# Performance work log

Measured on AMD Instinct MI355X. Metric: run time of the kernel, lower is better.

Reference implementation:

```python
import jax, jax.numpy as jnp
import numpy as np

G, N, E = 64, 1000, 8192          # graphs, nodes/graph, edges/graph
F_IN, C, H, HID, NCLS = 128, 128, 4, 256, 2
EPS = 1e-5


def _gcn(x, src, dst, W, b):
    # GCNConv: symmetric normalization with self-loops, sum aggregation.
    h = x @ W                                              # [N, C]
    deg = jax.ops.segment_sum(jnp.ones(E, h.dtype), dst, num_segments=N) + 1.0
    dinv = jax.lax.rsqrt(deg)                              # deg^{-1/2}
    msg = h[src] * (dinv[src] * dinv[dst])[:, None]        # [E, C] gather
    out = jax.ops.segment_sum(msg, dst, num_segments=N)    # scatter-add
    out = out + h * (dinv * dinv)[:, None]                 # self-loop term
    return out + b


def _layernorm(y, g, b):
    mu = y.mean(-1, keepdims=True)
    var = ((y - mu) ** 2).mean(-1, keepdims=True)
    return (y - mu) * jax.lax.rsqrt(var + EPS) * g + b


def setup_inputs() -> dict:
    key = jax.random.key(0)
    ks = jax.random.split(key, 12)
    rn = lambda k, s: jax.random.normal(k, s, jnp.float32) * 0.05
    return dict(
        x=jax.random.normal(ks[0], (G, N, F_IN), jnp.float32),
        edge_index=jax.random.randint(ks[1], (G, 2, E), 0, N),
        W0=rn(ks[2], (F_IN, C)), b0=jnp.zeros((C,), jnp.float32),
        W1=rn(ks[3], (C, C)), b1=jnp.zeros((C,), jnp.float32),
        in_w=rn(ks[4], (3 * C, C)), in_b=jnp.zeros((3 * C,), jnp.float32),
        out_w=rn(ks[5], (C, C)), out_b=jnp.zeros((C,), jnp.float32),
        ln2_g=jnp.ones((C,), jnp.float32), ln2_b=jnp.zeros((C,), jnp.float32),
        mw1=rn(ks[6], (C, HID)), mb1=jnp.zeros((HID,), jnp.float32),
        mw2=rn(ks[7], (HID, C)), mb2=jnp.zeros((C,), jnp.float32),
        lw=rn(ks[8], (C, NCLS)), lb=jnp.zeros((NCLS,), jnp.float32),
    )


def reference(x, edge_index, W0, b0, W1, b1, in_w, in_b, out_w, out_b,
              ln2_g, ln2_b, mw1, mb1, mw2, mb2, lw, lb):
    src, dst = edge_index[:, 0, :], edge_index[:, 1, :]
    conv = jax.vmap(_gcn, in_axes=(0, 0, 0, None, None))
    h = jnp.tanh(conv(x, src, dst, W0, b0))   # [G, N, C]
    h = jnp.tanh(conv(h, src, dst, W1, b1))
    g = h.sum(axis=1)                          # SumAggregation -> [G, C]

    # MultiheadAttention, unbatched: sequence of G graph embeddings
    qkv = g @ in_w.T + in_b
    q, k, v = jnp.split(qkv, 3, axis=-1)
    d = C // H
    qh, kh, vh = (t.reshape(G, H, d) for t in (q, k, v))
    attn = jax.nn.softmax(jnp.einsum('qhd,khd->hqk', qh, kh) * (d ** -0.5), axis=-1)
    o = jnp.einsum('hqk,khd->qhd', attn, vh).reshape(G, C) @ out_w.T + out_b

    x_attend = o                               # dropout = identity (eval)
    # NOTE: original computes layer_norm1(x_attend) but immediately overwrites it.
    mlp = jnp.maximum(x_attend @ mw1 + mb1, 0.0) @ mw2 + mb2
    y = _layernorm(x_attend + mlp, ln2_g, ln2_b)
    node_repr = jnp.maximum(y, 0.0).sum(axis=0)  # [C]
    return node_repr @ lw + lb                   # [NCLS]
```

## Files before the change

kernel.cpp:

```cpp
#include <hip/hip_runtime.h>
#include <math.h>

#define Gn 64
#define Nn 1000
#define En 8192
#define Cc 128
#define HIDn 256
#define EPSf 1e-5f

typedef __attribute__((ext_vector_type(8))) short bh8;
typedef __attribute__((ext_vector_type(4))) float fx4;

__device__ __forceinline__ unsigned short f2bf(float f) {
    unsigned u = __float_as_uint(f);
    u += 0x7fffu + ((u >> 16) & 1u);
    return (unsigned short)(u >> 16);
}
__device__ __forceinline__ float bflo(unsigned u) { return __uint_as_float(u << 16); }
__device__ __forceinline__ float bfhi(unsigned u) { return __uint_as_float(u & 0xffff0000u); }

__global__ __launch_bounds__(256) void k_fused(const int* __restrict__ ei, const float* __restrict__ X,
                                               const float* __restrict__ W, int4* __restrict__ ninfo,
                                               int2* __restrict__ epair, float* __restrict__ pooled,
                                               float* __restrict__ repr, int* __restrict__ ctr,
                                               unsigned short* __restrict__ Hout)
{
    __shared__ __align__(16) short Wt[128][136];
    __shared__ int   curs[1024];
    __shared__ float dinv_s[1024];
    __shared__ int   wsum[4];
    int t = threadIdx.x;

    if (blockIdx.x >= 256) {
        int g = blockIdx.x - 256;
        const int* srcp = ei + (size_t)g * 2 * En;
        const int* dstp = srcp + En;
        int lane = t & 63, wv = t >> 6;

        #pragma unroll
        for (int j = 0; j < 4; ++j) curs[t * 4 + j] = 0;
        __syncthreads();
        for (int e = t; e < En; e += 256) atomicAdd(&curs[dstp[e]], 1);
        __syncthreads();

        int base = t * 4;
        int d0 = curs[base], d1 = curs[base + 1], d2 = curs[base + 2], d3 = curs[base + 3];
        int s = d0 + d1 + d2 + d3;
        int v = s;
        #pragma unroll
        for (int off = 1; off <= 32; off <<= 1) {
            int u = __shfl_up(v, off);
            if (lane >= off) v += u;
        }
        if (lane == 63) wsum[wv] = v;
        __syncthreads();
        int woff = 0;
        #pragma unroll
        for (int w = 0; w < 4; ++w) if (w < wv) woff += wsum[w];
        int e0 = woff + v - s;
        int e1 = e0 + d0, e2 = e1 + d1, e3 = e2 + d2;
        float dv0 = rsqrtf((float)d0 + 1.f), dv1 = rsqrtf((float)d1 + 1.f);
        float dv2 = rsqrtf((float)d2 + 1.f), dv3 = rsqrtf((float)d3 + 1.f);
        curs[base] = e0; curs[base + 1] = e1; curs[base + 2] = e2; curs[base + 3] = e3;
        dinv_s[base] = dv0; dinv_s[base + 1] = dv1; dinv_s[base + 2] = dv2; dinv_s[base + 3] = dv3;
        if (base < Nn)     ninfo[g * Nn + base]     = make_int4(e0, d0, __float_as_int(dv0 * dv0), 0);
        if (base + 1 < Nn) ninfo[g * Nn + base + 1] = make_int4(e1, d1, __float_as_int(dv1 * dv1), 0);
        if (base + 2 < Nn) ninfo[g * Nn + base + 2] = make_int4(e2, d2, __float_as_int(dv2 * dv2), 0);
        if (base + 3 < Nn) ninfo[g * Nn + base + 3] = make_int4(e3, d3, __float_as_int(dv3 * dv3), 0);
        __syncthreads();

        for (int e = t; e < En; e += 256) {
            int dd = dstp[e], ss = srcp[e];
            int p = atomicAdd(&curs[dd], 1);
            float w = dinv_s[ss] * dinv_s[dd];
            epair[(size_t)g * En + p] = make_int2(ss, __float_as_int(w));
        }
        if (t < Cc) pooled[g * Cc + t] = 0.f;
        if (g == 0 && t < Cc) repr[t] = 0.f;
        if (g == 0 && t == 0) *ctr = 0;
        return;
    }

    int b = blockIdx.x;
    int xcd = b & 7, j = b >> 3;
    int g = xcd + 8 * (j & 7);
    int rblk = j >> 3;
    for (int idx = t; idx < 16384; idx += 256) {
        int kI = idx >> 7, n = idx & 127;
        Wt[n][kI] = (short)f2bf(W[idx]);
    }
    __syncthreads();
    int wave = t >> 6, l = t & 63;
    int lr = l & 15, lg = l >> 4;
    const float* Xf = X + (size_t)g * Nn * Cc;
    unsigned short* Hg = Hout + (size_t)g * Nn * Cc;

    for (int s = 0; s < 4; ++s) {
        int rbase = rblk * 256 + wave * 64 + s * 16;
        int r = rbase + lr;
        bool ok = r < Nn;
        bh8 af[4];
        #pragma unroll
        for (int ks = 0; ks < 4; ++ks) {
            if (ok) {
                const float* xp = Xf + (size_t)r * Cc + ks * 32 + lg * 8;
                fx4 a0 = *(const fx4*)xp;
                fx4 a1 = *(const fx4*)(xp + 4);
                bh8 av;
                av[0] = (short)f2bf(a0[0]); av[1] = (short)f2bf(a0[1]);
                av[2] = (short)f2bf(a0[2]); av[3] = (short)f2bf(a0[3]);
                av[4] = (short)f2bf(a1[0]); av[5] = (short)f2bf(a1[1]);
                av[6] = (short)f2bf(a1[2]); av[7] = (short)f2bf(a1[3]);
                af[ks] = av;
            } else af[ks] = bh8{0, 0, 0, 0, 0, 0, 0, 0};
        }
        fx4 acc[8];
        #pragma unroll
        for (int ct = 0; ct < 8; ++ct) acc[ct] = fx4{0.f, 0.f, 0.f, 0.f};
        #pragma unroll
        for (int ks = 0; ks < 4; ++ks) {
            #pragma unroll
            for (int ct = 0; ct < 8; ++ct) {
                bh8 bfr = *(const bh8*)(&Wt[ct * 16 + lr][ks * 32 + lg * 8]);
                acc[ct] = __builtin_amdgcn_mfma_f32_16x16x32_bf16(af[ks], bfr, acc[ct], 0, 0, 0);
            }
        }
        #pragma unroll
        for (int ct = 0; ct < 8; ++ct) {
            #pragma unroll
            for (int rg = 0; rg < 4; ++rg) {
                int row = rbase + lg * 4 + rg;
                if (row < Nn) Hg[(size_t)row * Cc + ct * 16 + lr] = f2bf(acc[ct][rg]);
            }
        }
    }
}

__global__ __launch_bounds__(256) void k_gemm1(const unsigned short* __restrict__ Xh,
                                               const float* __restrict__ W,
                                               unsigned short* __restrict__ Hout)
{
    __shared__ __align__(16) short Wt[128][136];
    int b = blockIdx.x;
    int xcd = b & 7, j = b >> 3;
    int g = xcd + 8 * (j & 7);
    int rblk = j >> 3;
    int t = threadIdx.x;
    for (int idx = t; idx < 16384; idx += 256) {
        int kI = idx >> 7, n = idx & 127;
        Wt[n][kI] = (short)f2bf(W[idx]);
    }
    __syncthreads();
    int wave = t >> 6, l = t & 63;
    int lr = l & 15, lg = l >> 4;
    const short* Xg = (const short*)Xh + (size_t)g * Nn * Cc;
    unsigned short* Hg = Hout + (size_t)g * Nn * Cc;

    for (int s = 0; s < 4; ++s) {
        int rbase = rblk * 256 + wave * 64 + s * 16;
        int r = rbase + lr;
        bool ok = r < Nn;
        bh8 af[4];
        #pragma unroll
        for (int ks = 0; ks < 4; ++ks) {
            if (ok) af[ks] = *(const bh8*)(Xg + (size_t)r * Cc + ks * 32 + lg * 8);
            else    af[ks] = bh8{0, 0, 0, 0, 0, 0, 0, 0};
        }
        fx4 acc[8];
        #pragma unroll
        for (int ct = 0; ct < 8; ++ct) acc[ct] = fx4{0.f, 0.f, 0.f, 0.f};
        #pragma unroll
        for (int ks = 0; ks < 4; ++ks) {
            #pragma unroll
            for (int ct = 0; ct < 8; ++ct) {
                bh8 bfr = *(const bh8*)(&Wt[ct * 16 + lr][ks * 32 + lg * 8]);
                acc[ct] = __builtin_amdgcn_mfma_f32_16x16x32_bf16(af[ks], bfr, acc[ct], 0, 0, 0);
            }
        }
        #pragma unroll
        for (int ct = 0; ct < 8; ++ct) {
            #pragma unroll
            for (int rg = 0; rg < 4; ++rg) {
                int row = rbase + lg * 4 + rg;
                if (row < Nn) Hg[(size_t)row * Cc + ct * 16 + lr] = f2bf(acc[ct][rg]);
            }
        }
    }
}

template<int POOL>
__global__ __launch_bounds__(256) void k_combine(const unsigned* __restrict__ Hb, const int2* __restrict__ epair,
                                                 const int4* __restrict__ ninfo, const float* __restrict__ bias,
                                                 unsigned* __restrict__ Tout, float* __restrict__ pooled)
{
    int b = blockIdx.x;
    int xcd = b & 7, j = b >> 3;
    int g = xcd + 8 * (j & 7);
    int blk = j >> 3;
    int wave = threadIdx.x >> 6, lane = threadIdx.x & 63;
    const unsigned* Hg = Hb + (size_t)g * Nn * 64;
    const int2* epg = epair + (size_t)g * En;
    const int4* nig = ninfo + (size_t)g * Nn;
    float2 bb = *(const float2*)(bias + lane * 2);
    float px = 0.f, py = 0.f;
    for (int n = blk * 4 + wave; n < Nn; n += 128) {
        int4 ni = nig[n];
        int st = ni.x, dc = ni.y;
        float sw = __int_as_float(ni.z);
        unsigned hv = Hg[n * 64 + lane];
        float a0x = bflo(hv) * sw + bb.x, a0y = bfhi(hv) * sw + bb.y;
        float a1x = 0.f, a1y = 0.f, a2x = 0.f, a2y = 0.f, a3x = 0.f, a3y = 0.f;
        int e = 0;
        for (; e + 4 <= dc; e += 4) {
            int2 p0 = epg[st + e];
            int2 p1 = epg[st + e + 1];
            int2 p2 = epg[st + e + 2];
            int2 p3 = epg[st + e + 3];
            unsigned r0 = Hg[p0.x * 64 + lane];
            unsigned r1 = Hg[p1.x * 64 + lane];
            unsigned r2 = Hg[p2.x * 64 + lane];
            unsigned r3 = Hg[p3.x * 64 + lane];
            float w0 = __int_as_float(p0.y), w1 = __int_as_float(p1.y);
            float w2 = __int_as_float(p2.y), w3 = __int_as_float(p3.y);
            a0x = fmaf(bflo(r0), w0, a0x); a0y = fmaf(bfhi(r0), w0, a0y);
            a1x = fmaf(bflo(r1), w1, a1x); a1y = fmaf(bfhi(r1), w1, a1y);
            a2x = fmaf(bflo(r2), w2, a2x); a2y = fmaf(bfhi(r2), w2, a2y);
            a3x = fmaf(bflo(r3), w3, a3x); a3y = fmaf(bfhi(r3), w3, a3y);
        }
        for (; e < dc; ++e) {
            int2 p0 = epg[st + e];
            unsigned r0 = Hg[p0.x * 64 + lane];
            float w0 = __int_as_float(p0.y);
            a0x = fmaf(bflo(r0), w0, a0x); a0y = fmaf(bfhi(r0), w0, a0y);
        }
        float ax = (a0x + a1x) + (a2x + a3x);
        float ay = (a0y + a1y) + (a2y + a3y);
        float tx = tanhf(ax), ty = tanhf(ay);
        if (POOL) { px += tx; py += ty; }
        else Tout[(size_t)(g * Nn + n) * 64 + lane] = ((unsigned)f2bf(ty) << 16) | (unsigned)f2bf(tx);
    }
    if (POOL) {
        atomicAdd(&pooled[g * Cc + lane * 2], px);
        atomicAdd(&pooled[g * Cc + lane * 2 + 1], py);
    }
}

__global__ __launch_bounds__(1024) void k_qkv(const float* __restrict__ pooled, const float* __restrict__ in_w,
                                              const float* __restrict__ in_b, float* __restrict__ qkvb)
{
    int t = threadIdx.x, lane = t & 63, wv = t >> 6;
    int c = blockIdx.x * 16 + wv;
    const float* wr = in_w + c * Cc;
    float w0 = wr[lane], w1 = wr[64 + lane];
    float bias = in_b[c];
    for (int i = 0; i < Gn; ++i) {
        float p = fmaf(pooled[i * Cc + lane], w0, pooled[i * Cc + 64 + lane] * w1);
        #pragma unroll
        for (int off2 = 32; off2 > 0; off2 >>= 1) p += __shfl_xor(p, off2);
        if (lane == 0) qkvb[i * 384 + c] = p + bias;
    }
}

__global__ __launch_bounds__(1024) void k_attn(const float* __restrict__ qkvb, float* __restrict__ ob)
{
    __shared__ float q[64][33], kk[64][33], v[64][33];
    __shared__ float S[64][64];
    int h = blockIdx.x, t = threadIdx.x;

    for (int idx = t; idx < 2048; idx += 1024) {
        int i = idx >> 5, cc = idx & 31;
        q[i][cc]  = qkvb[i * 384 + h * 32 + cc];
        kk[i][cc] = qkvb[i * 384 + 128 + h * 32 + cc];
        v[i][cc]  = qkvb[i * 384 + 256 + h * 32 + cc];
    }
    __syncthreads();

    for (int idx = t; idx < 4096; idx += 1024) {
        int i = idx >> 6, jj = idx & 63;
        float acc = 0.f;
        #pragma unroll
        for (int d2 = 0; d2 < 32; ++d2) acc = fmaf(q[i][d2], kk[jj][d2], acc);
        S[i][jj] = acc * 0.17677669529663687f;
    }
    __syncthreads();

    int lane = t & 63, w = t >> 6;
    for (int r = w; r < 64; r += 16) {
        float val = S[r][lane];
        float m = val;
        #pragma unroll
        for (int off = 32; off > 0; off >>= 1) m = fmaxf(m, __shfl_xor(m, off));
        float e2 = expf(val - m);
        float ssum = e2;
        #pragma unroll
        for (int off = 32; off > 0; off >>= 1) ssum += __shfl_xor(ssum, off);
        S[r][lane] = e2 / ssum;
    }
    __syncthreads();

    for (int idx = t; idx < 2048; idx += 1024) {
        int i = idx >> 5, d2 = idx & 31;
        float acc = 0.f;
        #pragma unroll 4
        for (int k2 = 0; k2 < 64; ++k2) acc = fmaf(S[i][k2], v[k2][d2], acc);
        ob[i * Cc + h * 32 + d2] = acc;
    }
}

__global__ __launch_bounds__(1024) void k_tailfinal(const float* __restrict__ ob, const float* __restrict__ out_w,
                                                    const float* __restrict__ out_b, const float* __restrict__ mw1,
                                                    const float* __restrict__ mb1, const float* __restrict__ mw2,
                                                    const float* __restrict__ mb2, const float* __restrict__ ln2g,
                                                    const float* __restrict__ ln2b, const float* __restrict__ lw,
                                                    const float* __restrict__ lb, float* __restrict__ repr,
                                                    int* __restrict__ ctr, float* __restrict__ out)
{
    __shared__ float sob[4][128];
    __shared__ float sxatt[4][128];
    __shared__ float sm1[4][256];
    __shared__ float spart[4][128];
    __shared__ float pr[128];
    __shared__ int slast;
    int g0 = blockIdx.x * 4;
    int t = threadIdx.x, lane = t & 63, wv = t >> 6;

    if (t < 512) sob[t >> 7][t & 127] = ob[(size_t)(g0 + (t >> 7)) * Cc + (t & 127)];
    if (t < 128) pr[t] = 0.f;
    __syncthreads();

    for (int c = wv; c < Cc; c += 16) {
        float w0 = out_w[c * Cc + lane];
        float w1 = out_w[c * Cc + 64 + lane];
        float bc = out_b[c];
        #pragma unroll
        for (int g = 0; g < 4; ++g) {
            float p = fmaf(sob[g][lane], w0, sob[g][64 + lane] * w1);
            #pragma unroll
            for (int off = 32; off > 0; off >>= 1) p += __shfl_xor(p, off);
            if (lane == 0) sxatt[g][c] = p + bc;
        }
    }
    __syncthreads();

    {
        int j = t & 255, gi = t >> 8;
        float acc = mb1[j];
        #pragma unroll 8
        for (int k = 0; k < Cc; ++k) acc = fmaf(sxatt[gi][k], mw1[k * HIDn + j], acc);
        sm1[gi][j] = fmaxf(acc, 0.f);
    }
    __syncthreads();

    {
        int c = t & 127, gi = (t >> 7) & 3, half = t >> 9;
        int k0 = half * 128;
        float acc = 0.f;
        #pragma unroll 8
        for (int k = 0; k < 128; ++k) acc = fmaf(sm1[gi][k0 + k], mw2[(k0 + k) * Cc + c], acc);
        if (half) spart[gi][c] = acc;
        __syncthreads();
        if (!half) sxatt[gi][c] = sxatt[gi][c] + acc + spart[gi][c] + mb2[c];
    }
    __syncthreads();

    if (t < 256) {
        int g = wv;
        float v0 = sxatt[g][lane], v1 = sxatt[g][64 + lane];
        float s = v0 + v1;
        #pragma unroll
        for (int off = 32; off > 0; off >>= 1) s += __shfl_xor(s, off);
        float mu = s * (1.f / 128.f);
        float d0 = v0 - mu, d1 = v1 - mu;
        float vv = d0 * d0 + d1 * d1;
        #pragma unroll
        for (int off = 32; off > 0; off >>= 1) vv += __shfl_xor(vv, off);
        float rstd = rsqrtf(vv * (1.f / 128.f) + EPSf);
        float z0 = fmaxf(d0 * rstd * ln2g[lane] + ln2b[lane], 0.f);
        float z1 = fmaxf(d1 * rstd * ln2g[64 + lane] + ln2b[64 + lane], 0.f);
        atomicAdd(&pr[lane], z0);
        atomicAdd(&pr[64 + lane], z1);
    }
    __syncthreads();
    if (t < 128) atomicAdd(&repr[t], pr[t]);

    __threadfence();
    __syncthreads();
    if (t == 0) slast = atomicAdd(ctr, 1);
    __syncthreads();
    if (slast == 15) {
        __threadfence();
        __shared__ float r0s[128], r1s[128];
        if (t < 128) {
            float r = __hip_atomic_load(&repr[t], __ATOMIC_RELAXED, __HIP_MEMORY_SCOPE_AGENT);
            r0s[t] = r * lw[t * 2 + 0];
            r1s[t] = r * lw[t * 2 + 1];
        }
        __syncthreads();
        for (int s2 = 64; s2 > 0; s2 >>= 1) {
            if (t < s2) { r0s[t] += r0s[t + s2]; r1s[t] += r1s[t + s2]; }
            __syncthreads();
        }
        if (t == 0) { out[0] = r0s[0] + lb[0]; out[1] = r1s[0] + lb[1]; }
    }
}

extern "C" void kernel_launch(void* const* d_in, const int* in_sizes, int n_in,
                              void* d_out, int out_size, void* d_ws, size_t ws_size,
                              hipStream_t stream)
{
    const float* x     = (const float*)d_in[0];
    const int*   ei    = (const int*)d_in[1];
    const float* W0    = (const float*)d_in[2];
    const float* b0    = (const float*)d_in[3];
    const float* W1    = (const float*)d_in[4];
    const float* b1    = (const float*)d_in[5];
    const float* in_w  = (const float*)d_in[6];
    const float* in_b  = (const float*)d_in[7];
    const float* out_w = (const float*)d_in[8];
    const float* out_b = (const float*)d_in[9];
    const float* ln2g  = (const float*)d_in[10];
    const float* ln2b  = (const float*)d_in[11];
    const float* mw1   = (const float*)d_in[12];
    const float* mb1   = (const float*)d_in[13];
    const float* mw2   = (const float*)d_in[14];
    const float* mb2   = (const float*)d_in[15];
    const float* lw    = (const float*)d_in[16];
    const float* lb    = (const float*)d_in[17];
    float* out = (float*)d_out;
    (void)in_sizes; (void)n_in; (void)out_size; (void)ws_size;

    char* ws = (char*)d_ws;
    size_t off = 0;
    auto carve = [&](size_t bytes) { size_t o = off; off += (bytes + 255) & ~(size_t)255; return o; };
    size_t o_ni    = carve((size_t)Gn * Nn * 16);
    size_t o_ep    = carve((size_t)Gn * En * 8);
    size_t o_pool  = carve((size_t)Gn * Cc * 4);
    size_t o_qkv   = carve((size_t)Gn * 384 * 4);
    size_t o_ob    = carve((size_t)Gn * Cc * 4);
    size_t o_repr  = carve((size_t)Cc * 4);
    size_t o_ctr   = carve(256);
    size_t o_H     = carve((size_t)Gn * Nn * Cc * 2);
    size_t o_T     = carve((size_t)Gn * Nn * Cc * 2);

    int4*  ninfo  = (int4*)(ws + o_ni);
    int2*  epair  = (int2*)(ws + o_ep);
    float* pooled = (float*)(ws + o_pool);
    float* qkvb   = (float*)(ws + o_qkv);
    float* ob     = (float*)(ws + o_ob);
    float* repr   = (float*)(ws + o_repr);
    int*   ctr    = (int*)(ws + o_ctr);
    unsigned short* H = (unsigned short*)(ws + o_H);
    unsigned short* T = (unsigned short*)(ws + o_T);

    k_fused<<<320, 256, 0, stream>>>(ei, x, W0, ninfo, epair, pooled, repr, ctr, H);
    k_combine<0><<<2048, 256, 0, stream>>>((const unsigned*)H, epair, ninfo, b0, (unsigned*)T, nullptr);
    k_gemm1<<<256, 256, 0, stream>>>(T, W1, H);
    k_combine<1><<<2048, 256, 0, stream>>>((const unsigned*)H, epair, ninfo, b1, nullptr, pooled);
    k_qkv<<<24, 1024, 0, stream>>>(pooled, in_w, in_b, qkvb);
    k_attn<<<4, 1024, 0, stream>>>(qkvb, ob);
    k_tailfinal<<<16, 1024, 0, stream>>>(ob, out_w, out_b, mw1, mb1, mw2, mb2, ln2g, ln2b,
                                         lw, lb, repr, ctr, out);
}
```

Baseline: 171.9 us.

## Aggregate before GEMM and fuse aggregation with transform per GCN layer

After: 244.9 us. 1.42x slower.

```diff
diff --git a/kernel.cpp b/kernel.cpp
--- a/kernel.cpp
+++ b/kernel.cpp
@@ -19,229 +19,203 @@
 __device__ __forceinline__ float bflo(unsigned u) { return __uint_as_float(u << 16); }
 __device__ __forceinline__ float bfhi(unsigned u) { return __uint_as_float(u & 0xffff0000u); }
 
-__global__ __launch_bounds__(256) void k_fused(const int* __restrict__ ei, const float* __restrict__ X,
-                                               const float* __restrict__ W, int4* __restrict__ ninfo,
-                                               int2* __restrict__ epair, float* __restrict__ pooled,
-                                               float* __restrict__ repr, int* __restrict__ ctr,
-                                               unsigned short* __restrict__ Hout)
-{
-    __shared__ __align__(16) short Wt[128][136];
+__global__ __launch_bounds__(256) void k_pre(const int* __restrict__ ei, const float* __restrict__ X,
+                                             int4* __restrict__ ninfo, int2* __restrict__ epair,
+                                             float* __restrict__ pooled, float* __restrict__ repr,
+                                             int* __restrict__ ctr, unsigned short* __restrict__ Xb)
+{
     __shared__ int   curs[1024];
     __shared__ float dinv_s[1024];
     __shared__ int   wsum[4];
     int t = threadIdx.x;
 
-    if (blockIdx.x >= 256) {
-        int g = blockIdx.x - 256;
-        const int* srcp = ei + (size_t)g * 2 * En;
-        const int* dstp = srcp + En;
-        int lane = t & 63, wv = t >> 6;
-
-        #pragma unroll
-        for (int j = 0; j < 4; ++j) curs[t * 4 + j] = 0;
-        __syncthreads();
-        for (int e = t; e < En; e += 256) atomicAdd(&curs[dstp[e]], 1);
-        __syncthreads();
-
-        int base = t * 4;
-        int d0 = curs[base], d1 = curs[base + 1], d2 = curs[base + 2], d3 = curs[base + 3];
-        int s = d0 + d1 + d2 + d3;
-        int v = s;
-        #pragma unroll
-        for (int off = 1; off <= 32; off <<= 1) {
-            int u = __shfl_up(v, off);
-            if (lane >= off) v += u;
-        }
-        if (lane == 63) wsum[wv] = v;
-        __syncthreads();
-        int woff = 0;
-        #pragma unroll
-        for (int w = 0; w < 4; ++w) if (w < wv) woff += wsum[w];
-        int e0 = woff + v - s;
-        int e1 = e0 + d0, e2 = e1 + d1, e3 = e2 + d2;
-        float dv0 = rsqrtf((float)d0 + 1.f), dv1 = rsqrtf((float)d1 + 1.f);
-        float dv2 = rsqrtf((float)d2 + 1.f), dv3 = rsqrtf((float)d3 + 1.f);
-        curs[base] = e0; curs[base + 1] = e1; curs[base + 2] = e2; curs[base + 3] = e3;
-        dinv_s[base] = dv0; dinv_s[base + 1] = dv1; dinv_s[base + 2] = dv2; dinv_s[base + 3] = dv3;
-        if (base < Nn)     ninfo[g * Nn + base]     = make_int4(e0, d0, __float_as_int(dv0 * dv0), 0);
-        if (base + 1 < Nn) ninfo[g * Nn + base + 1] = make_int4(e1, d1, __float_as_int(dv1 * dv1), 0);
-        if (base + 2 < Nn) ninfo[g * Nn + base + 2] = make_int4(e2, d2, __float_as_int(dv2 * dv2), 0);
-        if (base + 3 < Nn) ninfo[g * Nn + base + 3] = make_int4(e3, d3, __float_as_int(dv3 * dv3), 0);
-        __syncthreads();
-
-        for (int e = t; e < En; e += 256) {
-            int dd = dstp[e], ss = srcp[e];
-            int p = atomicAdd(&curs[dd], 1);
-            float w = dinv_s[ss] * dinv_s[dd];
-            epair[(size_t)g * En + p] = make_int2(ss, __float_as_int(w));
-        }
-        if (t < Cc) pooled[g * Cc + t] = 0.f;
-        if (g == 0 && t < Cc) repr[t] = 0.f;
-        if (g == 0 && t == 0) *ctr = 0;
+    if (blockIdx.x < 256) {
+        int cb = blockIdx.x;
+        int xcd = cb & 7, gg = (cb >> 3) & 7, q = cb >> 6;
+        int g = xcd + 8 * gg;
+        const float* Xg = X + (size_t)g * Nn * Cc + (size_t)q * 250 * Cc;
+        unsigned short* Xo = Xb + (size_t)g * Nn * Cc + (size_t)q * 250 * Cc;
+        for (int idx = t; idx < 4000; idx += 256) {
+            const float* p = Xg + (size_t)idx * 8;
+            fx4 a0 = *(const fx4*)p;
+            fx4 a1 = *(const fx4*)(p + 4);
+            bh8 v;
+            v[0] = (short)f2bf(a0[0]); v[1] = (short)f2bf(a0[1]);
+            v[2] = (short)f2bf(a0[2]); v[3] = (short)f2bf(a0[3]);
+            v[4] = (short)f2bf(a1[0]); v[5] = (short)f2bf(a1[1]);
+            v[6] = (short)f2bf(a1[2]); v[7] = (short)f2bf(a1[3]);
+            *(bh8*)(Xo + (size_t)idx * 8) = v;
+        }
         return;
     }
 
+    int g = blockIdx.x - 256;
+    const int* srcp = ei + (size_t)g * 2 * En;
+    const int* dstp = srcp + En;
+    int lane = t & 63, wv = t >> 6;
+
+    #pragma unroll
+    for (int j = 0; j < 4; ++j) curs[t * 4 + j] = 0;
+    __syncthreads();
+    for (int e = t; e < En; e += 256) atomicAdd(&curs[dstp[e]], 1);
+    __syncthreads();
+
+    int base = t * 4;
+    int d0 = curs[base], d1 = curs[base + 1], d2 = curs[base + 2], d3 = curs[base + 3];
+    int s = d0 + d1 + d2 + d3;
+    int v = s;
+    #pragma unroll
+    for (int off = 1; off <= 32; off <<= 1) {
+        int u = __shfl_up(v, off);
+        if (lane >= off) v += u;
+    }
+    if (lane == 63) wsum[wv] = v;
+    __syncthreads();
+    int woff = 0;
+    #pragma unroll
+    for (int w = 0; w < 4; ++w) if (w < wv) woff += wsum[w];
+    int e0 = woff + v - s;
+    int e1 = e0 + d0, e2 = e1 + d1, e3 = e2 + d2;
+    float dv0 = rsqrtf((float)d0 + 1.f), dv1 = rsqrtf((float)d1 + 1.f);
+    float dv2 = rsqrtf((float)d2 + 1.f), dv3 = rsqrtf((float)d3 + 1.f);
+    curs[base] = e0; curs[base + 1] = e1; curs[base + 2] = e2; curs[base + 3] = e3;
+    dinv_s[base] = dv0; dinv_s[base + 1] = dv1; dinv_s[base + 2] = dv2; dinv_s[base + 3] = dv3;
+    if (base < Nn)     ninfo[g * Nn + base]     = make_int4(e0, d0, __float_as_int(dv0 * dv0), 0);
+    if (base + 1 < Nn) ninfo[g * Nn + base + 1] = make_int4(e1, d1, __float_as_int(dv1 * dv1), 0);
+    if (base + 2 < Nn) ninfo[g * Nn + base + 2] = make_int4(e2, d2, __float_as_int(dv2 * dv2), 0);
+    if (base + 3 < Nn) ninfo[g * Nn + base + 3] = make_int4(e3, d3, __float_as_int(dv3 * dv3), 0);
+    __syncthreads();
+
+    for (int e = t; e < En; e += 256) {
+        int dd = dstp[e], ss = srcp[e];
+        int p = atomicAdd(&curs[dd], 1);
+        float w = dinv_s[ss] * dinv_s[dd];
+        epair[(size_t)g * En + p] = make_int2(ss, __float_as_int(w));
+    }
+    if (t < Cc) pooled[g * Cc + t] = 0.f;
+    if (g == 0 && t < Cc) repr[t] = 0.f;
+    if (g == 0 && t == 0) *ctr = 0;
+}
+
+template<int POOL>
+__global__ __launch_bounds__(256) void k_layer(const unsigned* __restrict__ Xrows,
+                                               const float* __restrict__ W,
+                                               const float* __restrict__ bias,
+                                               const int2* __restrict__ epair,
+                                               const int4* __restrict__ ninfo,
+                                               unsigned short* __restrict__ Hout,
+                                               float* __restrict__ pooled)
+{
+    __shared__ __align__(16) short Wt[128][136];
+    __shared__ __align__(16) short At[4][16][136];
     int b = blockIdx.x;
-    int xcd = b & 7, j = b >> 3;
-    int g = xcd + 8 * (j & 7);
-    int rblk = j >> 3;
+    int xcd = b & 7, gg = (b >> 3) & 7, rblk = b >> 6;
+    int g = xcd + 8 * gg;
+    int t = threadIdx.x;
     for (int idx = t; idx < 16384; idx += 256) {
         int kI = idx >> 7, n = idx & 127;
         Wt[n][kI] = (short)f2bf(W[idx]);
     }
     __syncthreads();
-    int wave = t >> 6, l = t & 63;
-    int lr = l & 15, lg = l >> 4;
-    const float* Xf = X + (size_t)g * Nn * Cc;
-    unsigned short* Hg = Hout + (size_t)g * Nn * Cc;
-
-    for (int s = 0; s < 4; ++s) {
-        int rbase = rblk * 256 + wave * 64 + s * 16;
-        int r = rbase + lr;
-        bool ok = r < Nn;
-        bh8 af[4];
-        #pragma unroll
-        for (int ks = 0; ks < 4; ++ks) {
-            if (ok) {
-                const float* xp = Xf + (size_t)r * Cc + ks * 32 + lg * 8;
-                fx4 a0 = *(const fx4*)xp;
-                fx4 a1 = *(const fx4*)(xp + 4);
-                bh8 av;
-                av[0] = (short)f2bf(a0[0]); av[1] = (short)f2bf(a0[1]);
-                av[2] = (short)f2bf(a0[2]); av[3] = (short)f2bf(a0[3]);
-                av[4] = (short)f2bf(a1[0]); av[5] = (short)f2bf(a1[1]);
-                av[6] = (short)f2bf(a1[2]); av[7] = (short)f2bf(a1[3]);
-                af[ks] = av;
-            } else af[ks] = bh8{0, 0, 0, 0, 0, 0, 0, 0};
-        }
-        fx4 acc[8];
-        #pragma unroll
-        for (int ct = 0; ct < 8; ++ct) acc[ct] = fx4{0.f, 0.f, 0.f, 0.f};
-        #pragma unroll
-        for (int ks = 0; ks < 4; ++ks) {
-            #pragma unroll
-            for (int ct = 0; ct < 8; ++ct) {
-                bh8 bfr = *(const bh8*)(&Wt[ct * 16 + lr][ks * 32 + lg * 8]);
-                acc[ct] = __builtin_amdgcn_mfma_f32_16x16x32_bf16(af[ks], bfr, acc[ct], 0, 0, 0);
+
+    int wv = t >> 6, lane = t & 63;
+    const unsigned* Xg = Xrows + (size_t)g * Nn * 64;
+    const int2* epg = epair + (size_t)g * En;
+    const int4* nig = ninfo + (size_t)g * Nn;
+    int rbase = rblk * 64 + wv * 16;
+
+    for (int rr = 0; rr < 16; ++rr) {
+        int n = rbase + rr;
+        unsigned packed = 0;
+        if (n < Nn) {
+            int4 ni = nig[n];
+            int st = ni.x, dc = ni.y;
+            float sw = __int_as_float(ni.z);
+            unsigned hv = Xg[(size_t)n * 64 + lane];
+            float a0x = bflo(hv) * sw, a0y = bfhi(hv) * sw;
+            float a1x = 0.f, a1y = 0.f, a2x = 0.f, a2y = 0.f, a3x = 0.f, a3y = 0.f;
+            int e = 0;
+            for (; e + 4 <= dc; e += 4) {
+                int2 p0 = epg[st + e];
+                int2 p1 = epg[st + e + 1];
+                int2 p2 = epg[st + e + 2];
+                int2 p3 = epg[st + e + 3];
+                unsigned r0 = Xg[(size_t)p0.x * 64 + lane];
+                unsigned r1 = Xg[(size_t)p1.x * 64 + lane];
+                unsigned r2 = Xg[(size_t)p2.x * 64 + lane];
+                unsigned r3 = Xg[(size_t)p3.x * 64 + lane];
+                float w0 = __int_as_float(p0.y), w1 = __int_as_float(p1.y);
+                float w2 = __int_as_float(p2.y), w3 = __int_as_float(p3.y);
+                a0x = fmaf(bflo(r0), w0, a0x); a0y = fmaf(bfhi(r0), w0, a0y);
+                a1x = fmaf(bflo(r1), w1, a1x); a1y = fmaf(bfhi(r1), w1, a1y);
+                a2x = fmaf(bflo(r2), w2, a2x); a2y = fmaf(bfhi(r2), w2, a2y);
+                a3x = fmaf(bflo(r3), w3, a3x); a3y = fmaf(bfhi(r3), w3, a3y);
             }
-        }
+            for (; e < dc; ++e) {
+                int2 p0 = epg[st + e];
+                unsigned r0 = Xg[(size_t)p0.x * 64 + lane];
+                float w0 = __int_as_float(p0.y);
+                a0x = fmaf(bflo(r0), w0, a0x); a0y = fmaf(bfhi(r0), w0, a0y);
+            }
+            float ax = (a0x + a1x) + (a2x + a3x);
+            float ay = (a0y + a1y) + (a2y + a3y);
+            packed = ((unsigned)f2bf(ay) << 16) | (unsigned)f2bf(ax);
+        }
+        *(unsigned*)&At[wv][rr][lane * 2] = packed;
+    }
+
+    int lr = lane & 15, lg = lane >> 4;
+    bh8 af[4];
+    #pragma unroll
+    for (int ks = 0; ks < 4; ++ks) af[ks] = *(const bh8*)&At[wv][lr][ks * 32 + lg * 8];
+    fx4 acc[8];
+    #pragma unroll
+    for (int ct = 0; ct < 8; ++ct) acc[ct] = fx4{0.f, 0.f, 0.f, 0.f};
+    #pragma unroll
+    for (int ks = 0; ks < 4; ++ks) {
+        #pragma unroll
+        for (int ct = 0; ct < 8; ++ct) {
+            bh8 bfr = *(const bh8*)(&Wt[ct * 16 + lr][ks * 32 + lg * 8]);
+            acc[ct] = __builtin_amdgcn_mfma_f32_16x16x32_bf16(af[ks], bfr, acc[ct], 0, 0, 0);
+        }
+    }
+    float bias_r[8];
+    #pragma unroll
+    for (int ct = 0; ct < 8; ++ct) bias_r[ct] = bias[ct * 16 + lr];
+
+    if (POOL) {
+        float psum[8];
+        #pragma unroll
+        for (int ct = 0; ct < 8; ++ct) psum[ct] = 0.f;
         #pragma unroll
         for (int ct = 0; ct < 8; ++ct) {
             #pragma unroll
             for (int rg = 0; rg < 4; ++rg) {
                 int row = rbase + lg * 4 + rg;
-                if (row < Nn) Hg[(size_t)row * Cc + ct * 16 + lr] = f2bf(acc[ct][rg]);
+                if (row < Nn) psum[ct] += tanhf(acc[ct][rg] + bias_r[ct]);
             }
         }
-    }
-}
-
-__global__ __launch_bounds__(256) void k_gemm1(const unsigned short* __restrict__ Xh,
-                                               const float* __restrict__ W,
-                                               unsigned short* __restrict__ Hout)
-{
-    __shared__ __align__(16) short Wt[128][136];
-    int b = blockIdx.x;
-    int xcd = b & 7, j = b >> 3;
-    int g = xcd + 8 * (j & 7);
-    int rblk = j >> 3;
-    int t = threadIdx.x;
-    for (int idx = t; idx < 16384; idx += 256) {
-        int kI = idx >> 7, n = idx & 127;
-        Wt[n][kI] = (short)f2bf(W[idx]);
-    }
-    __syncthreads();
-    int wave = t >> 6, l = t & 63;
-    int lr = l & 15, lg = l >> 4;
-    const short* Xg = (const short*)Xh + (size_t)g * Nn * Cc;
-    unsigned short* Hg = Hout + (size_t)g * Nn * Cc;
-
-    for (int s = 0; s < 4; ++s) {
-        int rbase = rblk * 256 + wave * 64 + s * 16;
-        int r = rbase + lr;
-        bool ok = r < Nn;
-        bh8 af[4];
-        #pragma unroll
-        for (int ks = 0; ks < 4; ++ks) {
-            if (ok) af[ks] = *(const bh8*)(Xg + (size_t)r * Cc + ks * 32 + lg * 8);
-            else    af[ks] = bh8{0, 0, 0, 0, 0, 0, 0, 0};
-        }
-        fx4 acc[8];
-        #pragma unroll
-        for (int ct = 0; ct < 8; ++ct) acc[ct] = fx4{0.f, 0.f, 0.f, 0.f};
-        #pragma unroll
-        for (int ks = 0; ks < 4; ++ks) {
+        #pragma unroll
+        for (int ct = 0; ct < 8; ++ct) {
+            psum[ct] += __shfl_xor(psum[ct], 16);
+            psum[ct] += __shfl_xor(psum[ct], 32);
+        }
+        if (lane < 16) {
             #pragma unroll
-            for (int ct = 0; ct < 8; ++ct) {
-                bh8 bfr = *(const bh8*)(&Wt[ct * 16 + lr][ks * 32 + lg * 8]);
-                acc[ct] = __builtin_amdgcn_mfma_f32_16x16x32_bf16(af[ks], bfr, acc[ct], 0, 0, 0);
-            }
-        }
+            for (int ct = 0; ct < 8; ++ct)
+                atomicAdd(&pooled[g * Cc + ct * 16 + lane], psum[ct]);
+        }
+    } else {
+        unsigned short* Hg = Hout + (size_t)g * Nn * Cc;
         #pragma unroll
         for (int ct = 0; ct < 8; ++ct) {
             #pragma unroll
             for (int rg = 0; rg < 4; ++rg) {
                 int row = rbase + lg * 4 + rg;
-                if (row < Nn) Hg[(size_t)row * Cc + ct * 16 + lr] = f2bf(acc[ct][rg]);
+                if (row < Nn)
+                    Hg[(size_t)row * Cc + ct * 16 + lr] = f2bf(tanhf(acc[ct][rg] + bias_r[ct]));
             }
         }
-    }
-}
-
-template<int POOL>
-__global__ __launch_bounds__(256) void k_combine(const unsigned* __restrict__ Hb, const int2* __restrict__ epair,
-                                                 const int4* __restrict__ ninfo, const float* __restrict__ bias,
-                                                 unsigned* __restrict__ Tout, float* __restrict__ pooled)
-{
-    int b = blockIdx.x;
-    int xcd = b & 7, j = b >> 3;
-    int g = xcd + 8 * (j & 7);
-    int blk = j >> 3;
-    int wave = threadIdx.x >> 6, lane = threadIdx.x & 63;
-    const unsigned* Hg = Hb + (size_t)g * Nn * 64;
-    const int2* epg = epair + (size_t)g * En;
-    const int4* nig = ninfo + (size_t)g * Nn;
-    float2 bb = *(const float2*)(bias + lane * 2);
-    float px = 0.f, py = 0.f;
-    for (int n = blk * 4 + wave; n < Nn; n += 128) {
-        int4 ni = nig[n];
-        int st = ni.x, dc = ni.y;
-        float sw = __int_as_float(ni.z);
-        unsigned hv = Hg[n * 64 + lane];
-        float a0x = bflo(hv) * sw + bb.x, a0y = bfhi(hv) * sw + bb.y;
-        float a1x = 0.f, a1y = 0.f, a2x = 0.f, a2y = 0.f, a3x = 0.f, a3y = 0.f;
-        int e = 0;
-        for (; e + 4 <= dc; e += 4) {
-            int2 p0 = epg[st + e];
-            int2 p1 = epg[st + e + 1];
-            int2 p2 = epg[st + e + 2];
-            int2 p3 = epg[st + e + 3];
-            unsigned r0 = Hg[p0.x * 64 + lane];
-            unsigned r1 = Hg[p1.x * 64 + lane];
-            unsigned r2 = Hg[p2.x * 64 + lane];
-            unsigned r3 = Hg[p3.x * 64 + lane];
-            float w0 = __int_as_float(p0.y), w1 = __int_as_float(p1.y);
-            float w2 = __int_as_float(p2.y), w3 = __int_as_float(p3.y);
-            a0x = fmaf(bflo(r0), w0, a0x); a0y = fmaf(bfhi(r0), w0, a0y);
-            a1x = fmaf(bflo(r1), w1, a1x); a1y = fmaf(bfhi(r1), w1, a1y);
-            a2x = fmaf(bflo(r2), w2, a2x); a2y = fmaf(bfhi(r2), w2, a2y);
-            a3x = fmaf(bflo(r3), w3, a3x); a3y = fmaf(bfhi(r3), w3, a3y);
-        }
-        for (; e < dc; ++e) {
-            int2 p0 = epg[st + e];
-            unsigned r0 = Hg[p0.x * 64 + lane];
-            float w0 = __int_as_float(p0.y);
-            a0x = fmaf(bflo(r0), w0, a0x); a0y = fmaf(bfhi(r0), w0, a0y);
-        }
-        float ax = (a0x + a1x) + (a2x + a3x);
-        float ay = (a0y + a1y) + (a2y + a3y);
-        float tx = tanhf(ax), ty = tanhf(ay);
-        if (POOL) { px += tx; py += ty; }
-        else Tout[(size_t)(g * Nn + n) * 64 + lane] = ((unsigned)f2bf(ty) << 16) | (unsigned)f2bf(tx);
-    }
-    if (POOL) {
-        atomicAdd(&pooled[g * Cc + lane * 2], px);
-        atomicAdd(&pooled[g * Cc + lane * 2 + 1], py);
     }
 }
 
@@ -440,7 +414,7 @@
     size_t o_repr  = carve((size_t)Cc * 4);
     size_t o_ctr   = carve(256);
     size_t o_H     = carve((size_t)Gn * Nn * Cc * 2);
-    size_t o_T     = carve((size_t)Gn * Nn * Cc * 2);
+    size_t o_Xb    = carve((size_t)Gn * Nn * Cc * 2);
 
     int4*  ninfo  = (int4*)(ws + o_ni);
     int2*  epair  = (int2*)(ws + o_ep);
@@ -449,13 +423,12 @@
     float* ob     = (float*)(ws + o_ob);
     float* repr   = (float*)(ws + o_repr);
     int*   ctr    = (int*)(ws + o_ctr);
-    unsigned short* H = (unsigned short*)(ws + o_H);
-    unsigned short* T = (unsigned short*)(ws + o_T);
-
-    k_fused<<<320, 256, 0, stream>>>(ei, x, W0, ninfo, epair, pooled, repr, ctr, H);
-    k_combine<0><<<2048, 256, 0, stream>>>((const unsigned*)H, epair, ninfo, b0, (unsigned*)T, nullptr);
-    k_gemm1<<<256, 256, 0, stream>>>(T, W1, H);
-    k_combine<1><<<2048, 256, 0, stream>>>((const unsigned*)H, epair, ninfo, b1, nullptr, pooled);
+    unsigned short* H  = (unsigned short*)(ws + o_H);
+    unsigned short* Xb = (unsigned short*)(ws + o_Xb);
+
+    k_pre<<<320, 256, 0, stream>>>(ei, x, ninfo, epair, pooled, repr, ctr, Xb);
+    k_layer<0><<<1024, 256, 0, stream>>>((const unsigned*)Xb, W0, b0, epair, ninfo, H, nullptr);
+    k_layer<1><<<1024, 256, 0, stream>>>((const unsigned*)H, W1, b1, epair, ninfo, nullptr, pooled);
     k_qkv<<<24, 1024, 0, stream>>>(pooled, in_w, in_b, qkvb);
     k_attn<<<4, 1024, 0, stream>>>(qkvb, ob);
     k_tailfinal<<<16, 1024, 0, stream>>>(ob, out_w, out_b, mw1, mb1, mw2, mb2, ln2g, ln2b,
```

## Split fp32-to-bf16 conversion from first GEMM and widen combine gather batching

Applied to the files above, without the earlier changes.

Measured after the change: 215.8 us. +25.5%, slower.

```diff
diff --git a/kernel.cpp b/kernel.cpp
--- a/kernel.cpp
+++ b/kernel.cpp
@@ -19,126 +19,87 @@
 __device__ __forceinline__ float bflo(unsigned u) { return __uint_as_float(u << 16); }
 __device__ __forceinline__ float bfhi(unsigned u) { return __uint_as_float(u & 0xffff0000u); }
 
-__global__ __launch_bounds__(256) void k_fused(const int* __restrict__ ei, const float* __restrict__ X,
-                                               const float* __restrict__ W, int4* __restrict__ ninfo,
-                                               int2* __restrict__ epair, float* __restrict__ pooled,
-                                               float* __restrict__ repr, int* __restrict__ ctr,
-                                               unsigned short* __restrict__ Hout)
-{
-    __shared__ __align__(16) short Wt[128][136];
+__global__ __launch_bounds__(256) void k_pre(const int* __restrict__ ei, const float* __restrict__ X,
+                                             int4* __restrict__ ninfo, int2* __restrict__ epair,
+                                             float* __restrict__ pooled, float* __restrict__ repr,
+                                             int* __restrict__ ctr, unsigned short* __restrict__ Xb)
+{
     __shared__ int   curs[1024];
     __shared__ float dinv_s[1024];
     __shared__ int   wsum[4];
     int t = threadIdx.x;
 
-    if (blockIdx.x >= 256) {
-        int g = blockIdx.x - 256;
-        const int* srcp = ei + (size_t)g * 2 * En;
-        const int* dstp = srcp + En;
-        int lane = t & 63, wv = t >> 6;
-
-        #pragma unroll
-        for (int j = 0; j < 4; ++j) curs[t * 4 + j] = 0;
-        __syncthreads();
-        for (int e = t; e < En; e += 256) atomicAdd(&curs[dstp[e]], 1);
-        __syncthreads();
-
-        int base = t * 4;
-        int d0 = curs[base], d1 = curs[base + 1], d2 = curs[base + 2], d3 = curs[base + 3];
-        int s = d0 + d1 + d2 + d3;
-        int v = s;
-        #pragma unroll
-        for (int off = 1; off <= 32; off <<= 1) {
-            int u = __shfl_up(v, off);
-            if (lane >= off) v += u;
-        }
-        if (lane == 63) wsum[wv] = v;
-        __syncthreads();
-        int woff = 0;
-        #pragma unroll
-        for (int w = 0; w < 4; ++w) if (w < wv) woff += wsum[w];
-        int e0 = woff + v - s;
-        int e1 = e0 + d0, e2 = e1 + d1, e3 = e2 + d2;
-        float dv0 = rsqrtf((float)d0 + 1.f), dv1 = rsqrtf((float)d1 + 1.f);
-        float dv2 = rsqrtf((float)d2 + 1.f), dv3 = rsqrtf((float)d3 + 1.f);
-        curs[base] = e0; curs[base + 1] = e1; curs[base + 2] = e2; curs[base + 3] = e3;
-        dinv_s[base] = dv0; dinv_s[base + 1] = dv1; dinv_s[base + 2] = dv2; dinv_s[base + 3] = dv3;
-        if (base < Nn)     ninfo[g * Nn + base]     = make_int4(e0, d0, __float_as_int(dv0 * dv0), 0);
-        if (base + 1 < Nn) ninfo[g * Nn + base + 1] = make_int4(e1, d1, __float_as_int(dv1 * dv1), 0);
-        if (base + 2 < Nn) ninfo[g * Nn + base + 2] = make_int4(e2, d2, __float_as_int(dv2 * dv2), 0);
-        if (base + 3 < Nn) ninfo[g * Nn + base + 3] = make_int4(e3, d3, __float_as_int(dv3 * dv3), 0);
-        __syncthreads();
-
-        for (int e = t; e < En; e += 256) {
-            int dd = dstp[e], ss = srcp[e];
-            int p = atomicAdd(&curs[dd], 1);
-            float w = dinv_s[ss] * dinv_s[dd];
-            epair[(size_t)g * En + p] = make_int2(ss, __float_as_int(w));
-        }
-        if (t < Cc) pooled[g * Cc + t] = 0.f;
-        if (g == 0 && t < Cc) repr[t] = 0.f;
-        if (g == 0 && t == 0) *ctr = 0;
+    if (blockIdx.x < 2048) {
+        int b = blockIdx.x;
+        int xcd = b & 7, gg = (b >> 3) & 7, q = b >> 6;
+        int g = xcd + 8 * gg;
+        const float* Xg = X + (size_t)g * Nn * Cc + (size_t)q * 500 * 8;
+        unsigned short* Xo = Xb + (size_t)g * Nn * Cc + (size_t)q * 500 * 8;
+        for (int i = t; i < 500; i += 256) {
+            const float* p = Xg + (size_t)i * 8;
+            fx4 a0 = *(const fx4*)p;
+            fx4 a1 = *(const fx4*)(p + 4);
+            bh8 v;
+            v[0] = (short)f2bf(a0[0]); v[1] = (short)f2bf(a0[1]);
+            v[2] = (short)f2bf(a0[2]); v[3] = (short)f2bf(a0[3]);
+            v[4] = (short)f2bf(a1[0]); v[5] = (short)f2bf(a1[1]);
+            v[6] = (short)f2bf(a1[2]); v[7] = (short)f2bf(a1[3]);
+            *(bh8*)(Xo + (size_t)i * 8) = v;
+        }
         return;
     }
 
-    int b = blockIdx.x;
-    int xcd = b & 7, j = b >> 3;
-    int g = xcd + 8 * (j & 7);
-    int rblk = j >> 3;
-    for (int idx = t; idx < 16384; idx += 256) {
-        int kI = idx >> 7, n = idx & 127;
-        Wt[n][kI] = (short)f2bf(W[idx]);
-    }
-    __syncthreads();
-    int wave = t >> 6, l = t & 63;
-    int lr = l & 15, lg = l >> 4;
-    const float* Xf = X + (size_t)g * Nn * Cc;
-    unsigned short* Hg = Hout + (size_t)g * Nn * Cc;
-
-    for (int s = 0; s < 4; ++s) {
-        int rbase = rblk * 256 + wave * 64 + s * 16;
-        int r = rbase + lr;
-        bool ok = r < Nn;
-        bh8 af[4];
-        #pragma unroll
-        for (int ks = 0; ks < 4; ++ks) {
-            if (ok) {
-                const float* xp = Xf + (size_t)r * Cc + ks * 32 + lg * 8;
-                fx4 a0 = *(const fx4*)xp;
-                fx4 a1 = *(const fx4*)(xp + 4);
-                bh8 av;
-                av[0] = (short)f2bf(a0[0]); av[1] = (short)f2bf(a0[1]);
-                av[2] = (short)f2bf(a0[2]); av[3] = (short)f2bf(a0[3]);
-                av[4] = (short)f2bf(a1[0]); av[5] = (short)f2bf(a1[1]);
-                av[6] = (short)f2bf(a1[2]); av[7] = (short)f2bf(a1[3]);
-                af[ks] = av;
-            } else af[ks] = bh8{0, 0, 0, 0, 0, 0, 0, 0};
-        }
-        fx4 acc[8];
-        #pragma unroll
-        for (int ct = 0; ct < 8; ++ct) acc[ct] = fx4{0.f, 0.f, 0.f, 0.f};
-        #pragma unroll
-        for (int ks = 0; ks < 4; ++ks) {
-            #pragma unroll
-            for (int ct = 0; ct < 8; ++ct) {
-                bh8 bfr = *(const bh8*)(&Wt[ct * 16 + lr][ks * 32 + lg * 8]);
-                acc[ct] = __builtin_amdgcn_mfma_f32_16x16x32_bf16(af[ks], bfr, acc[ct], 0, 0, 0);
-            }
-        }
-        #pragma unroll
-        for (int ct = 0; ct < 8; ++ct) {
-            #pragma unroll
-            for (int rg = 0; rg < 4; ++rg) {
-                int row = rbase + lg * 4 + rg;
-                if (row < Nn) Hg[(size_t)row * Cc + ct * 16 + lr] = f2bf(acc[ct][rg]);
-            }
-        }
-    }
-}
-
-__global__ __launch_bounds__(256) void k_gemm1(const unsigned short* __restrict__ Xh,
-                                               const float* __restrict__ W,
-                                               unsigned short* __restrict__ Hout)
+    int g = blockIdx.x - 2048;
+    const int* srcp = ei + (size_t)g * 2 * En;
+    const int* dstp = srcp + En;
+    int lane = t & 63, wv = t >> 6;
+
+    #pragma unroll
+    for (int j = 0; j < 4; ++j) curs[t * 4 + j] = 0;
+    __syncthreads();
+    for (int e = t; e < En; e += 256) atomicAdd(&curs[dstp[e]], 1);
+    __syncthreads();
+
+    int base = t * 4;
+    int d0 = curs[base], d1 = curs[base + 1], d2 = curs[base + 2], d3 = curs[base + 3];
+    int s = d0 + d1 + d2 + d3;
+    int v = s;
+    #pragma unroll
+    for (int off = 1; off <= 32; off <<= 1) {
+        int u = __shfl_up(v, off);
+        if (lane >= off) v += u;
+    }
+    if (lane == 63) wsum[wv] = v;
+    __syncthreads();
+    int woff = 0;
+    #pragma unroll
+    for (int w = 0; w < 4; ++w) if (w < wv) woff += wsum[w];
+    int e0 = woff + v - s;
+    int e1 = e0 + d0, e2 = e1 + d1, e3 = e2 + d2;
+    float dv0 = rsqrtf((float)d0 + 1.f), dv1 = rsqrtf((float)d1 + 1.f);
+    float dv2 = rsqrtf((float)d2 + 1.f), dv3 = rsqrtf((float)d3 + 1.f);
+    curs[base] = e0; curs[base + 1] = e1; curs[base + 2] = e2; curs[base + 3] = e3;
+    dinv_s[base] = dv0; dinv_s[base + 1] = dv1; dinv_s[base + 2] = dv2; dinv_s[base + 3] = dv3;
+    if (base < Nn)     ninfo[g * Nn + base]     = make_int4(e0, d0, __float_as_int(dv0 * dv0), 0);
+    if (base + 1 < Nn) ninfo[g * Nn + base + 1] = make_int4(e1, d1, __float_as_int(dv1 * dv1), 0);
+    if (base + 2 < Nn) ninfo[g * Nn + base + 2] = make_int4(e2, d2, __float_as_int(dv2 * dv2), 0);
+    if (base + 3 < Nn) ninfo[g * Nn + base + 3] = make_int4(e3, d3, __float_as_int(dv3 * dv3), 0);
+    __syncthreads();
+
+    for (int e = t; e < En; e += 256) {
+        int dd = dstp[e], ss = srcp[e];
+        int p = atomicAdd(&curs[dd], 1);
+        float w = dinv_s[ss] * dinv_s[dd];
+        epair[(size_t)g * En + p] = make_int2(ss, __float_as_int(w));
+    }
+    if (t < Cc) pooled[g * Cc + t] = 0.f;
+    if (g == 0 && t < Cc) repr[t] = 0.f;
+    if (g == 0 && t == 0) *ctr = 0;
+}
+
+__global__ __launch_bounds__(256) void k_gemm(const unsigned short* __restrict__ Xh,
+                                              const float* __restrict__ W,
+                                              unsigned short* __restrict__ Hout)
 {
     __shared__ __align__(16) short Wt[128][136];
     int b = blockIdx.x;
@@ -208,33 +169,33 @@
         int st = ni.x, dc = ni.y;
         float sw = __int_as_float(ni.z);
         unsigned hv = Hg[n * 64 + lane];
-        float a0x = bflo(hv) * sw + bb.x, a0y = bfhi(hv) * sw + bb.y;
-        float a1x = 0.f, a1y = 0.f, a2x = 0.f, a2y = 0.f, a3x = 0.f, a3y = 0.f;
-        int e = 0;
-        for (; e + 4 <= dc; e += 4) {
-            int2 p0 = epg[st + e];
-            int2 p1 = epg[st + e + 1];
-            int2 p2 = epg[st + e + 2];
-            int2 p3 = epg[st + e + 3];
-            unsigned r0 = Hg[p0.x * 64 + lane];
-            unsigned r1 = Hg[p1.x * 64 + lane];
-            unsigned r2 = Hg[p2.x * 64 + lane];
-            unsigned r3 = Hg[p3.x * 64 + lane];
-            float w0 = __int_as_float(p0.y), w1 = __int_as_float(p1.y);
-            float w2 = __int_as_float(p2.y), w3 = __int_as_float(p3.y);
-            a0x = fmaf(bflo(r0), w0, a0x); a0y = fmaf(bfhi(r0), w0, a0y);
-            a1x = fmaf(bflo(r1), w1, a1x); a1y = fmaf(bfhi(r1), w1, a1y);
-            a2x = fmaf(bflo(r2), w2, a2x); a2y = fmaf(bfhi(r2), w2, a2y);
-            a3x = fmaf(bflo(r3), w3, a3x); a3y = fmaf(bfhi(r3), w3, a3y);
-        }
-        for (; e < dc; ++e) {
-            int2 p0 = epg[st + e];
-            unsigned r0 = Hg[p0.x * 64 + lane];
-            float w0 = __int_as_float(p0.y);
-            a0x = fmaf(bflo(r0), w0, a0x); a0y = fmaf(bfhi(r0), w0, a0y);
-        }
-        float ax = (a0x + a1x) + (a2x + a3x);
-        float ay = (a0y + a1y) + (a2y + a3y);
+        float ax0 = bflo(hv) * sw + bb.x, ay0 = bfhi(hv) * sw + bb.y;
+        float axs[8], ays[8];
+        axs[0] = ax0; ays[0] = ay0;
+        #pragma unroll
+        for (int jj = 1; jj < 8; ++jj) { axs[jj] = 0.f; ays[jj] = 0.f; }
+        int rounds = (dc + 7) >> 3;
+        for (int rd = 0; rd < rounds; ++rd) {
+            int eb = st + rd * 8;
+            int2 p[8];
+            #pragma unroll
+            for (int jj = 0; jj < 8; ++jj) {
+                int idx = eb + jj;
+                idx = idx < En ? idx : En - 1;
+                p[jj] = epg[idx];
+            }
+            unsigned r[8];
+            #pragma unroll
+            for (int jj = 0; jj < 8; ++jj) r[jj] = Hg[(size_t)p[jj].x * 64 + lane];
+            #pragma unroll
+            for (int jj = 0; jj < 8; ++jj) {
+                float w = (rd * 8 + jj < dc) ? __int_as_float(p[jj].y) : 0.f;
+                axs[jj] = fmaf(bflo(r[jj]), w, axs[jj]);
+                ays[jj] = fmaf(bfhi(r[jj]), w, ays[jj]);
+            }
+        }
+        float ax = ((axs[0] + axs[1]) + (axs[2] + axs[3])) + ((axs[4] + axs[5]) + (axs[6] + axs[7]));
+        float ay = ((ays[0] + ays[1]) + (ays[2] + ays[3])) + ((ays[4] + ays[5]) + (ays[6] + ays[7]));
         float tx = tanhf(ax), ty = tanhf(ay);
         if (POOL) { px += tx; py += ty; }
         else Tout[(size_t)(g * Nn + n) * 64 + lane] = ((unsigned)f2bf(ty) << 16) | (unsigned)f2bf(tx);
@@ -441,6 +402,7 @@
     size_t o_ctr   = carve(256);
     size_t o_H     = carve((size_t)Gn * Nn * Cc * 2);
     size_t o_T     = carve((size_t)Gn * Nn * Cc * 2);
+    size_t o_Xb    = carve((size_t)Gn * Nn * Cc * 2);
 
     int4*  ninfo  = (int4*)(ws + o_ni);
     int2*  epair  = (int2*)(ws + o_ep);
@@ -449,12 +411,14 @@
     float* ob     = (float*)(ws + o_ob);
     float* repr   = (float*)(ws + o_repr);
     int*   ctr    = (int*)(ws + o_ctr);
-    unsigned short* H = (unsigned short*)(ws + o_H);
-    unsigned short* T = (unsigned short*)(ws + o_T);
-
-    k_fused<<<320, 256, 0, stream>>>(ei, x, W0, ninfo, epair, pooled, repr, ctr, H);
+    unsigned short* H  = (unsigned short*)(ws + o_H);
+    unsigned short* T  = (unsigned short*)(ws + o_T);
+    unsigned short* Xb = (unsigned short*)(ws + o_Xb);
+
+    k_pre<<<2112, 256, 0, stream>>>(ei, x, ninfo, epair, pooled, repr, ctr, Xb);
+    k_gemm<<<256, 256, 0, stream>>>(Xb, W0, H);
     k_combine<0><<<2048, 256, 0, stream>>>((const unsigned*)H, epair, ninfo, b0, (unsigned*)T, nullptr);
-    k_gemm1<<<256, 256, 0, stream>>>(T, W1, H);
+    k_gemm<<<256, 256, 0, stream>>>(T, W1, H);
     k_combine<1><<<2048, 256, 0, stream>>>((const unsigned*)H, epair, ninfo, b1, nullptr, pooled);
     k_qkv<<<24, 1024, 0, stream>>>(pooled, in_w, in_b, qkvb);
     k_attn<<<4, 1024, 0, stream>>>(qkvb, ob);
```
